# Kernel optimization log

Hardware: AMD Instinct MI355X
Metric: run time of the kernel (lower is better)

Reference implementation:

```python
import jax, jax.numpy as jnp
from jax import lax
import numpy as np

DIM = 8
C = 192
N = 198  # 2 special tokens + 14*14 patches (distilled=True)
B = 1024


def quick_gelu(x):
    return x * jax.nn.sigmoid(1.702 * x)


def setup_inputs() -> dict:
    key = jax.random.key(0)
    ks = jax.random.split(key, 7)
    return {
        "x": jax.random.normal(ks[0], (B, N, C), dtype=jnp.float32),
        "w_down": jax.random.normal(ks[1], (DIM, C), dtype=jnp.float32) * 0.05,
        "b_down": jnp.zeros((DIM,), dtype=jnp.float32),
        "conv_w": jax.random.normal(ks[2], (DIM, DIM, 3, 3), dtype=jnp.float32) * 0.05,
        "conv_b": jnp.zeros((DIM,), dtype=jnp.float32),
        "w_up": jax.random.normal(ks[3], (C, DIM), dtype=jnp.float32) * 0.05,
        "b_up": jnp.zeros((C,), dtype=jnp.float32),
    }


def _conv3x3(t, conv_w, conv_b):
    # t: [B, dim, H, W]; 3x3, stride 1, pad 1 (SAME)
    y = lax.conv_general_dilated(
        t, conv_w, window_strides=(1, 1), padding=((1, 1), (1, 1)),
        dimension_numbers=("NCHW", "OIHW", "NCHW"))
    return y + conv_b[None, :, None, None]


def reference(x, w_down, b_down, conv_w, conv_b, w_up, b_up):
    b, n, c = x.shape
    dim = w_down.shape[0]
    # down projection + QuickGELU
    d = quick_gelu(jnp.einsum("bnc,dc->bnd", x, w_down) + b_down)
    # patch tokens -> [B, dim, 14, 14] -> conv -> [B, 196, dim]
    x_patch = d[:, 2:].reshape(b, 14, 14, dim).transpose(0, 3, 1, 2)
    x_patch = _conv3x3(x_patch, conv_w, conv_b)
    x_patch = x_patch.transpose(0, 2, 3, 1).reshape(b, 14 * 14, dim)
    # cls token -> [B, dim, 1, 1] -> conv (only center tap contributes) -> [B, 1, dim]
    x_cls = d[:, :1].reshape(b, 1, 1, dim).transpose(0, 3, 1, 2)
    x_cls = _conv3x3(x_cls, conv_w, conv_b)
    x_cls = x_cls.transpose(0, 2, 3, 1).reshape(b, 1, dim)
    zero_dist = jnp.zeros_like(x_cls)
    d2 = jnp.concatenate([x_cls, zero_dist, x_patch], axis=1)
    d2 = quick_gelu(d2)  # dropout is identity in eval mode
    return jnp.einsum("bnd,cd->bnc", d2, w_up) + b_up
```

## Files before the change

### kernel.cpp

```cpp
#include <hip/hip_runtime.h>
#include <math.h>

#define NTOK 198
#define CCH  192

typedef float vf4 __attribute__((ext_vector_type(4)));

__device__ __forceinline__ float qgelu(float v) {
    return v / (1.0f + __expf(-1.702f * v));
}

__device__ __forceinline__ float dot8(const float4& a, const float4& wa,
                                      const float4& b, const float4& wb) {
    return a.x*wa.x + a.y*wa.y + a.z*wa.z + a.w*wa.w
         + b.x*wb.x + b.y*wb.y + b.z*wb.z + b.w*wb.w;
}

__global__ __launch_bounds__(512, 4) void convpass_fused(
    const float* __restrict__ x,
    const float* __restrict__ w_down,
    const float* __restrict__ b_down,
    const float* __restrict__ conv_w,
    const float* __restrict__ conv_b,
    const float* __restrict__ w_up,
    const float* __restrict__ b_up,
    float* __restrict__ out)
{
    const int b   = blockIdx.x;
    const int tid = threadIdx.x;

    __shared__ float s_d[NTOK * 8];
    __shared__ float s_d2[NTOK * 8];
    __shared__ float s_cw[576];
    __shared__ float s_cb[8];

    for (int t = tid; t < 576; t += 512) {
        const int kk = t >> 6, rem = t & 63, o = rem >> 3, i = rem & 7;
        s_cw[t] = conv_w[(o * 8 + i) * 9 + kk];
    }
    if (tid < 8) s_cb[tid] = conv_b[tid];

    {
        const int lane  = tid & 63;
        const int wv    = tid >> 6;
        const int chunk = lane >> 3;
        const int dim   = lane & 7;

        float wreg[24];
        {
            const float* wp = w_down + dim * CCH + chunk * 24;
            #pragma unroll
            for (int j = 0; j < 24; ++j) wreg[j] = wp[j];
        }
        const float bd  = b_down[dim];
        const float* xb = x + (size_t)b * NTOK * CCH + chunk * 24;

        #pragma unroll 1
        for (int i = 0; i < 25; ++i) {
            const int idx = i * 8 + wv;
            const bool valid = (idx < NTOK);
            const int n = valid ? idx : 0;
            const float* xr = xb + (size_t)n * CCH;
            float a0 = 0.f, a1 = 0.f;
            #pragma unroll
            for (int j = 0; j < 3; ++j) {
                const float4 xv = *(const float4*)(xr + j * 8);
                const float4 xw = *(const float4*)(xr + j * 8 + 4);
                a0 += xv.x*wreg[j*8]   + xv.y*wreg[j*8+1] + xv.z*wreg[j*8+2] + xv.w*wreg[j*8+3];
                a1 += xw.x*wreg[j*8+4] + xw.y*wreg[j*8+5] + xw.z*wreg[j*8+6] + xw.w*wreg[j*8+7];
            }
            float acc = a0 + a1;
            acc += __shfl_xor(acc, 8);
            acc += __shfl_xor(acc, 16);
            acc += __shfl_xor(acc, 32);
            if (valid && lane < 8) s_d[idx * 8 + dim] = qgelu(acc + bd);
        }
    }
    __syncthreads();

    for (int j = tid; j < NTOK * 8; j += 512) {
        const int n = j >> 3, o = j & 7;
        if (n == 1) {
            s_d2[j] = 0.0f;
        } else if (n == 0) {
            const float4 d0 = *(const float4*)&s_d[0];
            const float4 d1 = *(const float4*)&s_d[4];
            const float4 w0 = *(const float4*)&s_cw[4 * 64 + o * 8];
            const float4 w1 = *(const float4*)&s_cw[4 * 64 + o * 8 + 4];
            s_d2[j] = qgelu(s_cb[o] + dot8(d0, w0, d1, w1));
        } else {
            const int pos = n - 2, h = pos / 14, w = pos % 14;
            float acc = s_cb[o];
            #pragma unroll
            for (int dh = -1; dh <= 1; ++dh) {
                const int hh = h + dh;
                if (hh < 0 || hh > 13) continue;
                #pragma unroll
                for (int dw = -1; dw <= 1; ++dw) {
                    const int ww = w + dw;
                    if (ww < 0 || ww > 13) continue;
                    const int tok = 2 + hh * 14 + ww;
                    const int kk  = (dh + 1) * 3 + (dw + 1);
                    const float4 d0 = *(const float4*)&s_d[tok * 8];
                    const float4 d1 = *(const float4*)&s_d[tok * 8 + 4];
                    const float4 w0 = *(const float4*)&s_cw[kk * 64 + o * 8];
                    const float4 w1 = *(const float4*)&s_cw[kk * 64 + o * 8 + 4];
                    acc += dot8(d0, w0, d1, w1);
                }
            }
            s_d2[j] = qgelu(acc);
        }
    }
    __syncthreads();

    const int c4 = tid % 48;
    const int tl = tid / 48;
    if (tl < 10) {
        float w_r[4][8];
        #pragma unroll
        for (int cc = 0; cc < 4; ++cc) {
            const float4 wa = *(const float4*)(w_up + (c4 * 4 + cc) * 8);
            const float4 wb = *(const float4*)(w_up + (c4 * 4 + cc) * 8 + 4);
            w_r[cc][0] = wa.x; w_r[cc][1] = wa.y; w_r[cc][2] = wa.z; w_r[cc][3] = wa.w;
            w_r[cc][4] = wb.x; w_r[cc][5] = wb.y; w_r[cc][6] = wb.z; w_r[cc][7] = wb.w;
        }
        const float4 bu = *(const float4*)(b_up + c4 * 4);
        float* outb = out + (size_t)b * NTOK * CCH;
        #pragma unroll 1
        for (int nr = tl; nr < NTOK; nr += 10) {
            const float4 da = *(const float4*)&s_d2[nr * 8];
            const float4 dv = *(const float4*)&s_d2[nr * 8 + 4];
            float accs[4] = {bu.x, bu.y, bu.z, bu.w};
            #pragma unroll
            for (int cc = 0; cc < 4; ++cc) {
                accs[cc] += da.x * w_r[cc][0] + da.y * w_r[cc][1]
                          + da.z * w_r[cc][2] + da.w * w_r[cc][3]
                          + dv.x * w_r[cc][4] + dv.y * w_r[cc][5]
                          + dv.z * w_r[cc][6] + dv.w * w_r[cc][7];
            }
            const vf4 r = {accs[0], accs[1], accs[2], accs[3]};
            __builtin_nontemporal_store(r, (vf4*)(outb + (size_t)nr * CCH + c4 * 4));
        }
    }
}

extern "C" void kernel_launch(void* const* d_in, const int* in_sizes, int n_in,
                              void* d_out, int out_size, void* d_ws, size_t ws_size,
                              hipStream_t stream) {
    const float* x      = (const float*)d_in[0];
    const float* w_down = (const float*)d_in[1];
    const float* b_down = (const float*)d_in[2];
    const float* conv_w = (const float*)d_in[3];
    const float* conv_b = (const float*)d_in[4];
    const float* w_up   = (const float*)d_in[5];
    const float* b_up   = (const float*)d_in[6];
    float* out = (float*)d_out;

    const int B = in_sizes[0] / (NTOK * CCH);
    convpass_fused<<<dim3(B), dim3(512), 0, stream>>>(
        x, w_down, b_down, conv_w, conv_b, w_up, b_up, out);
}
```

Before: 76.96 us.

## Split fused kernel into down-projection kernel and conv+up-projection kernel

The single fused kernel is split in two. The first runs the down projection and QuickGELU over all rows with a fixed grid of 2048 blocks and writes the 8-dim activations to workspace. The second loads those into shared memory and performs the conv and up projection. This decouples the read-heavy phase from the write-heavy phase so each can get its own occupancy and memory streaming behaviour. The cost is an extra launch and a small workspace round trip.

```diff
diff --git a/kernel.cpp b/kernel.cpp
--- a/kernel.cpp
+++ b/kernel.cpp
@@ -16,10 +16,52 @@
          + b.x*wb.x + b.y*wb.y + b.z*wb.z + b.w*wb.w;
 }
 
-__global__ __launch_bounds__(512, 4) void convpass_fused(
+__global__ __launch_bounds__(256, 4) void k1_down(
     const float* __restrict__ x,
     const float* __restrict__ w_down,
     const float* __restrict__ b_down,
+    float* __restrict__ d,
+    int n_rows, int rows_per_wave)
+{
+    const int lane  = threadIdx.x & 63;
+    const int chunk = lane >> 3;
+    const int dim   = lane & 7;
+    const int wid   = blockIdx.x * 4 + (threadIdx.x >> 6);
+
+    float wreg[24];
+    {
+        const float* wp = w_down + dim * CCH + chunk * 24;
+        #pragma unroll
+        for (int j = 0; j < 24; ++j) wreg[j] = wp[j];
+    }
+    const float bd = b_down[dim];
+    const float* xc = x + chunk * 24;
+
+    const int r0 = wid * rows_per_wave;
+    #pragma unroll 1
+    for (int i = 0; i < rows_per_wave; ++i) {
+        const int row = r0 + i;
+        const bool valid = (row < n_rows);
+        const int rs = valid ? row : 0;
+        const float* xr = xc + (size_t)rs * CCH;
+        float a0 = 0.f, a1 = 0.f;
+        #pragma unroll
+        for (int j = 0; j < 3; ++j) {
+            const float4 xv = *(const float4*)(xr + j * 8);
+            const float4 xw = *(const float4*)(xr + j * 8 + 4);
+            a0 += xv.x*wreg[j*8]   + xv.y*wreg[j*8+1] + xv.z*wreg[j*8+2] + xv.w*wreg[j*8+3];
+            a1 += xw.x*wreg[j*8+4] + xw.y*wreg[j*8+5] + xw.z*wreg[j*8+6] + xw.w*wreg[j*8+7];
+        }
+        float acc = a0 + a1;
+        acc += __shfl_xor(acc, 8);
+        acc += __shfl_xor(acc, 16);
+        acc += __shfl_xor(acc, 32);
+        if (valid && lane < 8) d[(size_t)row * 8 + dim] = qgelu(acc + bd);
+    }
+}
+
+__global__ __launch_bounds__(512, 4) void k2_conv_up(
+    const float* __restrict__ d,
     const float* __restrict__ conv_w,
     const float* __restrict__ conv_b,
     const float* __restrict__ w_up,
@@ -34,48 +76,16 @@
     __shared__ float s_cw[576];
     __shared__ float s_cb[8];
 
+    {
+        const float4* db4 = (const float4*)(d + (size_t)b * NTOK * 8);
+        for (int t = tid; t < NTOK * 2; t += 512)
+            *(float4*)&s_d[t * 4] = db4[t];
+    }
     for (int t = tid; t < 576; t += 512) {
         const int kk = t >> 6, rem = t & 63, o = rem >> 3, i = rem & 7;
         s_cw[t] = conv_w[(o * 8 + i) * 9 + kk];
     }
     if (tid < 8) s_cb[tid] = conv_b[tid];
-
-    {
-        const int lane  = tid & 63;
-        const int wv    = tid >> 6;
-        const int chunk = lane >> 3;
-        const int dim   = lane & 7;
-
-        float wreg[24];
-        {
-            const float* wp = w_down + dim * CCH + chunk * 24;
-            #pragma unroll
-            for (int j = 0; j < 24; ++j) wreg[j] = wp[j];
-        }
-        const float bd  = b_down[dim];
-        const float* xb = x + (size_t)b * NTOK * CCH + chunk * 24;
-
-        #pragma unroll 1
-        for (int i = 0; i < 25; ++i) {
-            const int idx = i * 8 + wv;
-            const bool valid = (idx < NTOK);
-            const int n = valid ? idx : 0;
-            const float* xr = xb + (size_t)n * CCH;
-            float a0 = 0.f, a1 = 0.f;
-            #pragma unroll
-            for (int j = 0; j < 3; ++j) {
-                const float4 xv = *(const float4*)(xr + j * 8);
-                const float4 xw = *(const float4*)(xr + j * 8 + 4);
-                a0 += xv.x*wreg[j*8]   + xv.y*wreg[j*8+1] + xv.z*wreg[j*8+2] + xv.w*wreg[j*8+3];
-                a1 += xw.x*wreg[j*8+4] + xw.y*wreg[j*8+5] + xw.z*wreg[j*8+6] + xw.w*wreg[j*8+7];
-            }
-            float acc = a0 + a1;
-            acc += __shfl_xor(acc, 8);
-            acc += __shfl_xor(acc, 16);
-            acc += __shfl_xor(acc, 32);
-            if (valid && lane < 8) s_d[idx * 8 + dim] = qgelu(acc + bd);
-        }
-    }
     __syncthreads();
 
     for (int j = tid; j < NTOK * 8; j += 512) {
@@ -157,6 +167,13 @@
     float* out = (float*)d_out;
 
     const int B = in_sizes[0] / (NTOK * CCH);
-    convpass_fused<<<dim3(B), dim3(512), 0, stream>>>(
-        x, w_down, b_down, conv_w, conv_b, w_up, b_up, out);
+    const int n_rows = B * NTOK;
+    const int k1_blocks = 2048;
+    const int n_waves = k1_blocks * 4;
+    const int rows_per_wave = (n_rows + n_waves - 1) / n_waves;
+
+    float* dbuf = (float*)d_ws;
+    k1_down<<<dim3(k1_blocks), dim3(256), 0, stream>>>(x, w_down, b_down, dbuf,
+                                                       n_rows, rows_per_wave);
+    k2_conv_up<<<dim3(B), dim3(512), 0, stream>>>(dbuf, conv_w, conv_b, w_up, b_up, out);
 }
```

Result: slower. 83.57 us (+8.6%).
